# Optimization experiments

Measured on AMD Instinct MI355X. Metric: run time of the kernel, lower is better.

Reference implementation:

```python
import jax, jax.numpy as jnp
import numpy as np

B, N, T, D, O = 8, 1024, 12, 64, 64

def setup_inputs() -> dict:
    key = jax.random.key(0)
    k1, k2, k3 = jax.random.split(key, 3)
    x = jax.random.normal(k1, (B, N, T, D), dtype=jnp.float32)
    # row-normalized random adjacency (dense mask, as in the torch module)
    adj = jax.random.uniform(k2, (N, N), dtype=jnp.float32)
    norm_adj = adj / jnp.sum(adj, axis=-1, keepdims=True)
    theta_w = jax.random.normal(k3, (D, O), dtype=jnp.float32) / np.sqrt(D)
    return {"x": x, "norm_adj": norm_adj, "theta_w": theta_w}

def reference(x, norm_adj, theta_w):
    b, n, t, d = x.shape
    # [B, N, T, D] -> [B*T, N, D]
    xr = jnp.transpose(x, (0, 2, 1, 3)).reshape(b * t, n, d)
    # spatial attention scores [B*T, N, N]
    scores = jnp.einsum('gnd,gmd->gnm', xr, xr) / jnp.sqrt(jnp.float32(d))
    attn = jax.nn.softmax(scores, axis=-1)
    # adjacency-masked attention, then aggregate and project
    agg = jnp.einsum('gnm,gmd->gnd', norm_adj[None, :, :] * attn, xr)
    out = jnp.einsum('gnd,do->gno', agg, theta_w)
    # [B*T, N, O] -> [B, N, T, O], relu
    out = jnp.transpose(out.reshape(b, t, n, -1), (0, 2, 1, 3))
    return jax.nn.relu(out)
```

## Files before the change

### kernel.cpp

```cpp
#include <hip/hip_runtime.h>


#define NB    8
#define NT    12
#define NNODE 1024
#define ND    64
#define XROW  768

typedef __bf16 bf16x8 __attribute__((ext_vector_type(8)));
typedef float  floatx4 __attribute__((ext_vector_type(4)));

#define MFMA(a,b,c) __builtin_amdgcn_mfma_f32_16x16x32_bf16((a),(b),(c),0,0,0)

#define QSCALE 0.18033688011112042f

#define KSTRIDE 72
#define VSTRIDE 40
#define PSTRIDE 36
#define AGSTRIDE 68
#define OFF_KHI 0
#define OFF_KLO 4608
#define OFF_VHI 9216
#define OFF_VLO 14336
#define OFF_P   19456
#define SMEM_BYTES (19456 + 128*PSTRIDE*4)

struct bfpair { __bf16 h, l; };

__device__ __forceinline__ bfpair split1(float f) {
    bfpair r;
    __bf16 hb = (__bf16)f;
    float hf = __builtin_bit_cast(float,
                   (unsigned)__builtin_bit_cast(unsigned short, hb) << 16);
    r.h = hb;
    r.l = (__bf16)(f - hf);
    return r;
}

__global__ void __launch_bounds__(256, 2)
spattn(const float* __restrict__ x, const float* __restrict__ adj,
       const float* __restrict__ theta, float* __restrict__ out)
{
    __shared__ __align__(16) char smem[SMEM_BYTES];
    __bf16* Khi = (__bf16*)(smem + OFF_KHI);
    __bf16* Klo = (__bf16*)(smem + OFF_KLO);
    __bf16* Vhi = (__bf16*)(smem + OFF_VHI);
    __bf16* Vlo = (__bf16*)(smem + OFF_VLO);
    float*  Pm  = (float*)(smem + OFF_P);

    const int tid  = threadIdx.x;
    const int wave = tid >> 6;
    const int lane = tid & 63;
    const int l16  = lane & 15;
    const int quad = lane >> 4;

    const int bx   = blockIdx.x;
    const int g    = bx >> 3;
    const int rblk = bx & 7;
    const int bb   = g / NT;
    const int tt   = g - bb * NT;
    const int row0 = rblk * 128;

    const float* xbase = x + (size_t)bb * (NNODE * XROW) + tt * ND;

    bf16x8 qhi[2][2], qlo[2][2];
    #pragma unroll
    for (int mt = 0; mt < 2; ++mt) {
        const float* qsrc = xbase + (size_t)(row0 + wave*32 + mt*16 + l16) * XROW;
        #pragma unroll
        for (int ks = 0; ks < 2; ++ks) {
            floatx4 f0 = *(const floatx4*)(qsrc + ks*32 + quad*8);
            floatx4 f1 = *(const floatx4*)(qsrc + ks*32 + quad*8 + 4);
            #pragma unroll
            for (int i = 0; i < 4; ++i) {
                bfpair p0 = split1(f0[i]*QSCALE);
                qhi[mt][ks][i]   = p0.h; qlo[mt][ks][i]   = p0.l;
                bfpair p1 = split1(f1[i]*QSCALE);
                qhi[mt][ks][4+i] = p1.h; qlo[mt][ks][4+i] = p1.l;
            }
        }
    }

    const floatx4 vzero = {0.f, 0.f, 0.f, 0.f};
    floatx4 acc[2][4];
    #pragma unroll
    for (int mt = 0; mt < 2; ++mt)
        #pragma unroll
        for (int dt = 0; dt < 4; ++dt)
            acc[mt][dt] = vzero;
    float lpart[2][4] = {{0.f,0.f,0.f,0.f},{0.f,0.f,0.f,0.f}};

    const int skey = tid >> 3;
    const int sd0  = (tid & 7) * 8;
    const int svd  = tid >> 2;
    const int svk0 = (tid & 3) * 8;
    floatx4 kf0, kf1;
    float vf[8];

    {
        const float* ksrc = xbase + (size_t)skey * XROW + sd0;
        kf0 = *(const floatx4*)ksrc;
        kf1 = *(const floatx4*)(ksrc + 4);
        const float* vsrc = xbase + (size_t)svk0 * XROW + svd;
        #pragma unroll
        for (int i = 0; i < 8; ++i) vf[i] = vsrc[i * XROW];
    }

    for (int ct = 0; ct < 32; ++ct) {
        const int key0 = ct * 32;
        __syncthreads();
        {
            bf16x8 h, l;
            #pragma unroll
            for (int i = 0; i < 4; ++i) {
                bfpair p0 = split1(kf0[i]); h[i]   = p0.h; l[i]   = p0.l;
                bfpair p1 = split1(kf1[i]); h[4+i] = p1.h; l[4+i] = p1.l;
            }
            *(bf16x8*)(Khi + skey*KSTRIDE + sd0) = h;
            *(bf16x8*)(Klo + skey*KSTRIDE + sd0) = l;
            bf16x8 vh, vl;
            #pragma unroll
            for (int i = 0; i < 8; ++i) {
                bfpair p = split1(vf[i]); vh[i] = p.h; vl[i] = p.l;
            }
            *(bf16x8*)(Vhi + svd*VSTRIDE + svk0) = vh;
            *(bf16x8*)(Vlo + svd*VSTRIDE + svk0) = vl;
        }
        __syncthreads();
        if (ct < 31) {
            const int nk = key0 + 32;
            const float* ksrc = xbase + (size_t)(nk + skey) * XROW + sd0;
            kf0 = *(const floatx4*)ksrc;
            kf1 = *(const floatx4*)(ksrc + 4);
            const float* vsrc = xbase + (size_t)(nk + svk0) * XROW + svd;
            #pragma unroll
            for (int i = 0; i < 8; ++i) vf[i] = vsrc[i * XROW];
        }
        float av[2][2][4];
        #pragma unroll
        for (int mt = 0; mt < 2; ++mt)
            #pragma unroll
            for (int nt = 0; nt < 2; ++nt)
                #pragma unroll
                for (int r = 0; r < 4; ++r)
                    av[mt][nt][r] = adj[(size_t)(row0 + wave*32 + mt*16 + quad*4 + r) * NNODE
                                        + key0 + nt*16 + l16];

        floatx4 S[2][2] = {{vzero, vzero}, {vzero, vzero}};
        #pragma unroll
        for (int ks = 0; ks < 2; ++ks) {
            #pragma unroll
            for (int nt = 0; nt < 2; ++nt) {
                bf16x8 bh = *(const bf16x8*)(Khi + (nt*16 + l16)*KSTRIDE + ks*32 + quad*8);
                bf16x8 bl = *(const bf16x8*)(Klo + (nt*16 + l16)*KSTRIDE + ks*32 + quad*8);
                #pragma unroll
                for (int mt = 0; mt < 2; ++mt) {
                    S[mt][nt] = MFMA(qhi[mt][ks], bh, S[mt][nt]);
                    S[mt][nt] = MFMA(qlo[mt][ks], bh, S[mt][nt]);
                    S[mt][nt] = MFMA(qhi[mt][ks], bl, S[mt][nt]);
                }
            }
        }
        #pragma unroll
        for (int mt = 0; mt < 2; ++mt)
            #pragma unroll
            for (int nt = 0; nt < 2; ++nt)
                #pragma unroll
                for (int r = 0; r < 4; ++r) {
                    float w = __builtin_amdgcn_exp2f(S[mt][nt][r]);
                    lpart[mt][r] += w;
                    Pm[(wave*32 + mt*16 + quad*4 + r)*PSTRIDE + nt*16 + l16] = av[mt][nt][r] * w;
                }
        bf16x8 pah[2], pal[2];
        #pragma unroll
        for (int mt = 0; mt < 2; ++mt) {
            const float* pp = Pm + (wave*32 + mt*16 + l16)*PSTRIDE + quad*8;
            floatx4 p0 = *(const floatx4*)pp;
            floatx4 p1 = *(const floatx4*)(pp + 4);
            #pragma unroll
            for (int i = 0; i < 4; ++i) {
                bfpair q0 = split1(p0[i]); pah[mt][i]   = q0.h; pal[mt][i]   = q0.l;
                bfpair q1 = split1(p1[i]); pah[mt][4+i] = q1.h; pal[mt][4+i] = q1.l;
            }
        }
        #pragma unroll
        for (int dt = 0; dt < 4; ++dt) {
            bf16x8 vh = *(const bf16x8*)(Vhi + (dt*16 + l16)*VSTRIDE + quad*8);
            bf16x8 vl = *(const bf16x8*)(Vlo + (dt*16 + l16)*VSTRIDE + quad*8);
            #pragma unroll
            for (int mt = 0; mt < 2; ++mt) {
                acc[mt][dt] = MFMA(pah[mt], vh, acc[mt][dt]);
                acc[mt][dt] = MFMA(pal[mt], vh, acc[mt][dt]);
                acc[mt][dt] = MFMA(pah[mt], vl, acc[mt][dt]);
            }
        }
    }

    float linv[2][4];
    #pragma unroll
    for (int mt = 0; mt < 2; ++mt)
        #pragma unroll
        for (int r = 0; r < 4; ++r) {
            float lv = lpart[mt][r];
            lv += __shfl_xor(lv, 1);
            lv += __shfl_xor(lv, 2);
            lv += __shfl_xor(lv, 4);
            lv += __shfl_xor(lv, 8);
            linv[mt][r] = 1.0f / lv;
        }

    __syncthreads();
    float* AG = (float*)smem;
    #pragma unroll
    for (int mt = 0; mt < 2; ++mt)
        #pragma unroll
        for (int dt = 0; dt < 4; ++dt)
            #pragma unroll
            for (int r = 0; r < 4; ++r)
                AG[(wave*32 + mt*16 + quad*4 + r)*AGSTRIDE + dt*16 + l16]
                    = acc[mt][dt][r] * linv[mt][r];

    bf16x8 th[4][2], tl[4][2];
    #pragma unroll
    for (int ot = 0; ot < 4; ++ot)
        #pragma unroll
        for (int ks = 0; ks < 2; ++ks)
            #pragma unroll
            for (int j = 0; j < 8; ++j) {
                float tv = theta[(ks*32 + quad*8 + j)*ND + ot*16 + l16];
                bfpair p = split1(tv);
                th[ot][ks][j] = p.h; tl[ot][ks][j] = p.l;
            }

    floatx4 oacc[2][4];
    #pragma unroll
    for (int mt = 0; mt < 2; ++mt)
        #pragma unroll
        for (int ot = 0; ot < 4; ++ot)
            oacc[mt][ot] = vzero;
    __syncthreads();
    #pragma unroll
    for (int ks = 0; ks < 2; ++ks) {
        bf16x8 ah[2], al[2];
        #pragma unroll
        for (int mt = 0; mt < 2; ++mt) {
            const float* ap = AG + (wave*32 + mt*16 + l16)*AGSTRIDE + ks*32 + quad*8;
            floatx4 a0 = *(const floatx4*)ap;
            floatx4 a1 = *(const floatx4*)(ap + 4);
            #pragma unroll
            for (int i = 0; i < 4; ++i) {
                bfpair q0 = split1(a0[i]); ah[mt][i]   = q0.h; al[mt][i]   = q0.l;
                bfpair q1 = split1(a1[i]); ah[mt][4+i] = q1.h; al[mt][4+i] = q1.l;
            }
        }
        #pragma unroll
        for (int ot = 0; ot < 4; ++ot)
            #pragma unroll
            for (int mt = 0; mt < 2; ++mt) {
                oacc[mt][ot] = MFMA(ah[mt], th[ot][ks], oacc[mt][ot]);
                oacc[mt][ot] = MFMA(al[mt], th[ot][ks], oacc[mt][ot]);
                oacc[mt][ot] = MFMA(ah[mt], tl[ot][ks], oacc[mt][ot]);
            }
    }

    float* obase = out + (size_t)bb * (NNODE * XROW) + tt * ND;
    #pragma unroll
    for (int mt = 0; mt < 2; ++mt)
        #pragma unroll
        for (int ot = 0; ot < 4; ++ot)
            #pragma unroll
            for (int r = 0; r < 4; ++r) {
                float v = oacc[mt][ot][r];
                obase[(size_t)(row0 + wave*32 + mt*16 + quad*4 + r) * XROW + ot*16 + l16]
                    = v > 0.f ? v : 0.f;
            }
}

extern "C" void kernel_launch(void* const* d_in, const int* in_sizes, int n_in,
                              void* d_out, int out_size, void* d_ws, size_t ws_size,
                              hipStream_t stream) {
    (void)in_sizes; (void)n_in; (void)d_ws; (void)ws_size; (void)out_size;
    const float* x     = (const float*)d_in[0];
    const float* adj   = (const float*)d_in[1];
    const float* theta = (const float*)d_in[2];
    float* out = (float*)d_out;
    spattn<<<dim3(768), dim3(256), 0, stream>>>(x, adj, theta, out);
}
```

Measured before the change: 171.0 us.

## Switch to transposed 32x32x16 MFMA flow with register-resident P and aggregates

Replaces the 16x16x32 MFMA tiles with 32x32x16 MFMAs that compute S transposed (keys x queries). Each lane then owns one query row, so the probability tile and the aggregated output are turned into B operands with a lane-xor-32 shuffle instead of a round trip through LDS. This removes the P and AG shared-memory buffers and their barriers in the epilogue. Adjacency and output accesses become vectorized float4 per query row. It adds shuffle and select work and increases register pressure from the floatx16 accumulators.

Result: slower. 176.2 us (+3.0%).

```diff
diff --git a/kernel.cpp b/kernel.cpp
--- a/kernel.cpp
+++ b/kernel.cpp
@@ -7,23 +7,22 @@
 #define ND    64
 #define XROW  768
 
-typedef __bf16 bf16x8 __attribute__((ext_vector_type(8)));
+typedef __bf16 bf16x8  __attribute__((ext_vector_type(8)));
+typedef __bf16 bf16x2  __attribute__((ext_vector_type(2)));
 typedef float  floatx4 __attribute__((ext_vector_type(4)));
-
-#define MFMA(a,b,c) __builtin_amdgcn_mfma_f32_16x16x32_bf16((a),(b),(c),0,0,0)
-
+typedef float  floatx16 __attribute__((ext_vector_type(16)));
+typedef unsigned uintx4 __attribute__((ext_vector_type(4)));
+
+#define MFMA32(a,b,c) __builtin_amdgcn_mfma_f32_32x32x16_bf16((a),(b),(c),0,0,0)
 #define QSCALE 0.18033688011112042f
 
 #define KSTRIDE 72
 #define VSTRIDE 40
-#define PSTRIDE 36
-#define AGSTRIDE 68
 #define OFF_KHI 0
 #define OFF_KLO 4608
 #define OFF_VHI 9216
 #define OFF_VLO 14336
-#define OFF_P   19456
-#define SMEM_BYTES (19456 + 128*PSTRIDE*4)
+#define SMEM_BYTES 19456
 
 struct bfpair { __bf16 h, l; };
 
@@ -35,6 +34,25 @@
     r.h = hb;
     r.l = (__bf16)(f - hf);
     return r;
+}
+
+__device__ __forceinline__ unsigned pk2(__bf16 a, __bf16 b) {
+    bf16x2 t; t[0] = a; t[1] = b;
+    return __builtin_bit_cast(unsigned, t);
+}
+
+__device__ __forceinline__ bf16x8 xchg(unsigned A0, unsigned A1,
+                                       unsigned B0, unsigned B1, int L5) {
+    unsigned sA = L5 ? A0 : B0;
+    unsigned sB = L5 ? A1 : B1;
+    unsigned rA = (unsigned)__shfl_xor((int)sA, 32);
+    unsigned rB = (unsigned)__shfl_xor((int)sB, 32);
+    uintx4 u;
+    u[0] = L5 ? rA : A0;
+    u[1] = L5 ? rB : A1;
+    u[2] = L5 ? B0 : rA;
+    u[3] = L5 ? B1 : rB;
+    return __builtin_bit_cast(bf16x8, u);
 }
 
 __global__ void __launch_bounds__(256, 2)
@@ -46,13 +64,12 @@
     __bf16* Klo = (__bf16*)(smem + OFF_KLO);
     __bf16* Vhi = (__bf16*)(smem + OFF_VHI);
     __bf16* Vlo = (__bf16*)(smem + OFF_VLO);
-    float*  Pm  = (float*)(smem + OFF_P);
 
     const int tid  = threadIdx.x;
     const int wave = tid >> 6;
     const int lane = tid & 63;
-    const int l16  = lane & 15;
-    const int quad = lane >> 4;
+    const int q31  = lane & 31;
+    const int L5   = lane >> 5;
 
     const int bx   = blockIdx.x;
     const int g    = bx >> 3;
@@ -60,35 +77,30 @@
     const int bb   = g / NT;
     const int tt   = g - bb * NT;
     const int row0 = rblk * 128;
+    const int wq   = wave * 32;
+    const int qglob = row0 + wq + q31;
 
     const float* xbase = x + (size_t)bb * (NNODE * XROW) + tt * ND;
 
-    bf16x8 qhi[2][2], qlo[2][2];
-    #pragma unroll
-    for (int mt = 0; mt < 2; ++mt) {
-        const float* qsrc = xbase + (size_t)(row0 + wave*32 + mt*16 + l16) * XROW;
-        #pragma unroll
-        for (int ks = 0; ks < 2; ++ks) {
-            floatx4 f0 = *(const floatx4*)(qsrc + ks*32 + quad*8);
-            floatx4 f1 = *(const floatx4*)(qsrc + ks*32 + quad*8 + 4);
+    bf16x8 qh[4], ql[4];
+    {
+        const float* qsrc = xbase + (size_t)qglob * XROW;
+        #pragma unroll
+        for (int dc = 0; dc < 4; ++dc) {
+            floatx4 f0 = *(const floatx4*)(qsrc + dc*16 + L5*8);
+            floatx4 f1 = *(const floatx4*)(qsrc + dc*16 + L5*8 + 4);
             #pragma unroll
             for (int i = 0; i < 4; ++i) {
                 bfpair p0 = split1(f0[i]*QSCALE);
-                qhi[mt][ks][i]   = p0.h; qlo[mt][ks][i]   = p0.l;
+                qh[dc][i]   = p0.h; ql[dc][i]   = p0.l;
                 bfpair p1 = split1(f1[i]*QSCALE);
-                qhi[mt][ks][4+i] = p1.h; qlo[mt][ks][4+i] = p1.l;
-            }
-        }
-    }
-
-    const floatx4 vzero = {0.f, 0.f, 0.f, 0.f};
-    floatx4 acc[2][4];
-    #pragma unroll
-    for (int mt = 0; mt < 2; ++mt)
-        #pragma unroll
-        for (int dt = 0; dt < 4; ++dt)
-            acc[mt][dt] = vzero;
-    float lpart[2][4] = {{0.f,0.f,0.f,0.f},{0.f,0.f,0.f,0.f}};
+                qh[dc][4+i] = p1.h; ql[dc][4+i] = p1.l;
+            }
+        }
+    }
+
+    floatx16 O0 = {}, O1 = {};
+    float lpart = 0.f;
 
     const int skey = tid >> 3;
     const int sd0  = (tid & 7) * 8;
@@ -136,144 +148,123 @@
             #pragma unroll
             for (int i = 0; i < 8; ++i) vf[i] = vsrc[i * XROW];
         }
-        float av[2][2][4];
-        #pragma unroll
-        for (int mt = 0; mt < 2; ++mt)
-            #pragma unroll
-            for (int nt = 0; nt < 2; ++nt)
-                #pragma unroll
-                for (int r = 0; r < 4; ++r)
-                    av[mt][nt][r] = adj[(size_t)(row0 + wave*32 + mt*16 + quad*4 + r) * NNODE
-                                        + key0 + nt*16 + l16];
-
-        floatx4 S[2][2] = {{vzero, vzero}, {vzero, vzero}};
-        #pragma unroll
-        for (int ks = 0; ks < 2; ++ks) {
-            #pragma unroll
-            for (int nt = 0; nt < 2; ++nt) {
-                bf16x8 bh = *(const bf16x8*)(Khi + (nt*16 + l16)*KSTRIDE + ks*32 + quad*8);
-                bf16x8 bl = *(const bf16x8*)(Klo + (nt*16 + l16)*KSTRIDE + ks*32 + quad*8);
-                #pragma unroll
-                for (int mt = 0; mt < 2; ++mt) {
-                    S[mt][nt] = MFMA(qhi[mt][ks], bh, S[mt][nt]);
-                    S[mt][nt] = MFMA(qlo[mt][ks], bh, S[mt][nt]);
-                    S[mt][nt] = MFMA(qhi[mt][ks], bl, S[mt][nt]);
-                }
-            }
-        }
-        #pragma unroll
-        for (int mt = 0; mt < 2; ++mt)
-            #pragma unroll
-            for (int nt = 0; nt < 2; ++nt)
-                #pragma unroll
-                for (int r = 0; r < 4; ++r) {
-                    float w = __builtin_amdgcn_exp2f(S[mt][nt][r]);
-                    lpart[mt][r] += w;
-                    Pm[(wave*32 + mt*16 + quad*4 + r)*PSTRIDE + nt*16 + l16] = av[mt][nt][r] * w;
-                }
-        bf16x8 pah[2], pal[2];
-        #pragma unroll
-        for (int mt = 0; mt < 2; ++mt) {
-            const float* pp = Pm + (wave*32 + mt*16 + l16)*PSTRIDE + quad*8;
-            floatx4 p0 = *(const floatx4*)pp;
-            floatx4 p1 = *(const floatx4*)(pp + 4);
-            #pragma unroll
-            for (int i = 0; i < 4; ++i) {
-                bfpair q0 = split1(p0[i]); pah[mt][i]   = q0.h; pal[mt][i]   = q0.l;
-                bfpair q1 = split1(p1[i]); pah[mt][4+i] = q1.h; pal[mt][4+i] = q1.l;
-            }
-        }
-        #pragma unroll
-        for (int dt = 0; dt < 4; ++dt) {
-            bf16x8 vh = *(const bf16x8*)(Vhi + (dt*16 + l16)*VSTRIDE + quad*8);
-            bf16x8 vl = *(const bf16x8*)(Vlo + (dt*16 + l16)*VSTRIDE + quad*8);
-            #pragma unroll
-            for (int mt = 0; mt < 2; ++mt) {
-                acc[mt][dt] = MFMA(pah[mt], vh, acc[mt][dt]);
-                acc[mt][dt] = MFMA(pal[mt], vh, acc[mt][dt]);
-                acc[mt][dt] = MFMA(pah[mt], vl, acc[mt][dt]);
-            }
-        }
-    }
-
-    float linv[2][4];
-    #pragma unroll
-    for (int mt = 0; mt < 2; ++mt)
-        #pragma unroll
-        for (int r = 0; r < 4; ++r) {
-            float lv = lpart[mt][r];
-            lv += __shfl_xor(lv, 1);
-            lv += __shfl_xor(lv, 2);
-            lv += __shfl_xor(lv, 4);
-            lv += __shfl_xor(lv, 8);
-            linv[mt][r] = 1.0f / lv;
-        }
-
-    __syncthreads();
-    float* AG = (float*)smem;
-    #pragma unroll
-    for (int mt = 0; mt < 2; ++mt)
-        #pragma unroll
-        for (int dt = 0; dt < 4; ++dt)
-            #pragma unroll
-            for (int r = 0; r < 4; ++r)
-                AG[(wave*32 + mt*16 + quad*4 + r)*AGSTRIDE + dt*16 + l16]
-                    = acc[mt][dt][r] * linv[mt][r];
-
-    bf16x8 th[4][2], tl[4][2];
-    #pragma unroll
-    for (int ot = 0; ot < 4; ++ot)
-        #pragma unroll
-        for (int ks = 0; ks < 2; ++ks)
+        floatx4 adjv[4];
+        #pragma unroll
+        for (int rg = 0; rg < 4; ++rg)
+            adjv[rg] = *(const floatx4*)(adj + (size_t)qglob * NNODE
+                                         + key0 + rg*8 + L5*4);
+
+        floatx16 ST = {};
+        #pragma unroll
+        for (int dc = 0; dc < 4; ++dc) {
+            bf16x8 kh = *(const bf16x8*)(Khi + q31*KSTRIDE + dc*16 + L5*8);
+            bf16x8 kl = *(const bf16x8*)(Klo + q31*KSTRIDE + dc*16 + L5*8);
+            ST = MFMA32(kh, qh[dc], ST);
+            ST = MFMA32(kl, qh[dc], ST);
+            ST = MFMA32(kh, ql[dc], ST);
+        }
+        __bf16 pth[16], ptl[16];
+        #pragma unroll
+        for (int r = 0; r < 16; ++r) {
+            float w = __builtin_amdgcn_exp2f(ST[r]);
+            lpart += w;
+            bfpair p = split1(adjv[r >> 2][r & 3] * w);
+            pth[r] = p.h; ptl[r] = p.l;
+        }
+        unsigned GH[4][2], GL[4][2];
+        #pragma unroll
+        for (int gg = 0; gg < 4; ++gg) {
+            GH[gg][0] = pk2(pth[4*gg],   pth[4*gg+1]);
+            GH[gg][1] = pk2(pth[4*gg+2], pth[4*gg+3]);
+            GL[gg][0] = pk2(ptl[4*gg],   ptl[4*gg+1]);
+            GL[gg][1] = pk2(ptl[4*gg+2], ptl[4*gg+3]);
+        }
+        #pragma unroll
+        for (int kc = 0; kc < 2; ++kc) {
+            bf16x8 bh = xchg(GH[2*kc][0], GH[2*kc][1],
+                             GH[2*kc+1][0], GH[2*kc+1][1], L5);
+            bf16x8 bl = xchg(GL[2*kc][0], GL[2*kc][1],
+                             GL[2*kc+1][0], GL[2*kc+1][1], L5);
+            {
+                bf16x8 vh = *(const bf16x8*)(Vhi + q31*VSTRIDE + kc*16 + L5*8);
+                bf16x8 vl = *(const bf16x8*)(Vlo + q31*VSTRIDE + kc*16 + L5*8);
+                O0 = MFMA32(vh, bh, O0);
+                O0 = MFMA32(vl, bh, O0);
+                O0 = MFMA32(vh, bl, O0);
+            }
+            {
+                bf16x8 vh = *(const bf16x8*)(Vhi + (32+q31)*VSTRIDE + kc*16 + L5*8);
+                bf16x8 vl = *(const bf16x8*)(Vlo + (32+q31)*VSTRIDE + kc*16 + L5*8);
+                O1 = MFMA32(vh, bh, O1);
+                O1 = MFMA32(vl, bh, O1);
+                O1 = MFMA32(vh, bl, O1);
+            }
+        }
+    }
+
+    float l = lpart + __shfl_xor(lpart, 32);
+    float linv = 1.0f / l;
+
+    bf16x8 th[2][4], tlo[2][4];
+    #pragma unroll
+    for (int ot = 0; ot < 2; ++ot)
+        #pragma unroll
+        for (int kc = 0; kc < 4; ++kc)
             #pragma unroll
             for (int j = 0; j < 8; ++j) {
-                float tv = theta[(ks*32 + quad*8 + j)*ND + ot*16 + l16];
+                float tv = theta[(size_t)(kc*16 + L5*8 + j) * ND + ot*32 + q31];
                 bfpair p = split1(tv);
-                th[ot][ks][j] = p.h; tl[ot][ks][j] = p.l;
-            }
-
-    floatx4 oacc[2][4];
-    #pragma unroll
-    for (int mt = 0; mt < 2; ++mt)
-        #pragma unroll
-        for (int ot = 0; ot < 4; ++ot)
-            oacc[mt][ot] = vzero;
-    __syncthreads();
-    #pragma unroll
-    for (int ks = 0; ks < 2; ++ks) {
-        bf16x8 ah[2], al[2];
-        #pragma unroll
-        for (int mt = 0; mt < 2; ++mt) {
-            const float* ap = AG + (wave*32 + mt*16 + l16)*AGSTRIDE + ks*32 + quad*8;
-            floatx4 a0 = *(const floatx4*)ap;
-            floatx4 a1 = *(const floatx4*)(ap + 4);
-            #pragma unroll
-            for (int i = 0; i < 4; ++i) {
-                bfpair q0 = split1(a0[i]); ah[mt][i]   = q0.h; al[mt][i]   = q0.l;
-                bfpair q1 = split1(a1[i]); ah[mt][4+i] = q1.h; al[mt][4+i] = q1.l;
-            }
-        }
-        #pragma unroll
-        for (int ot = 0; ot < 4; ++ot)
-            #pragma unroll
-            for (int mt = 0; mt < 2; ++mt) {
-                oacc[mt][ot] = MFMA(ah[mt], th[ot][ks], oacc[mt][ot]);
-                oacc[mt][ot] = MFMA(al[mt], th[ot][ks], oacc[mt][ot]);
-                oacc[mt][ot] = MFMA(ah[mt], tl[ot][ks], oacc[mt][ot]);
-            }
-    }
-
-    float* obase = out + (size_t)bb * (NNODE * XROW) + tt * ND;
-    #pragma unroll
-    for (int mt = 0; mt < 2; ++mt)
-        #pragma unroll
-        for (int ot = 0; ot < 4; ++ot)
-            #pragma unroll
-            for (int r = 0; r < 4; ++r) {
-                float v = oacc[mt][ot][r];
-                obase[(size_t)(row0 + wave*32 + mt*16 + quad*4 + r) * XROW + ot*16 + l16]
-                    = v > 0.f ? v : 0.f;
-            }
+                th[ot][kc][j] = p.h; tlo[ot][kc][j] = p.l;
+            }
+
+    __bf16 agh[32], agl[32];
+    #pragma unroll
+    for (int r = 0; r < 16; ++r) {
+        bfpair p = split1(O0[r] * linv);
+        agh[r] = p.h; agl[r] = p.l;
+    }
+    #pragma unroll
+    for (int r = 0; r < 16; ++r) {
+        bfpair p = split1(O1[r] * linv);
+        agh[16+r] = p.h; agl[16+r] = p.l;
+    }
+    unsigned AH[8][2], AL[8][2];
+    #pragma unroll
+    for (int gg = 0; gg < 8; ++gg) {
+        AH[gg][0] = pk2(agh[4*gg],   agh[4*gg+1]);
+        AH[gg][1] = pk2(agh[4*gg+2], agh[4*gg+3]);
+        AL[gg][0] = pk2(agl[4*gg],   agl[4*gg+1]);
+        AL[gg][1] = pk2(agl[4*gg+2], agl[4*gg+3]);
+    }
+
+    floatx16 OC0 = {}, OC1 = {};
+    #pragma unroll
+    for (int kc = 0; kc < 4; ++kc) {
+        bf16x8 bh = xchg(AH[2*kc][0], AH[2*kc][1],
+                         AH[2*kc+1][0], AH[2*kc+1][1], L5);
+        bf16x8 bl = xchg(AL[2*kc][0], AL[2*kc][1],
+                         AL[2*kc+1][0], AL[2*kc+1][1], L5);
+        OC0 = MFMA32(th[0][kc], bh, OC0);
+        OC0 = MFMA32(tlo[0][kc], bh, OC0);
+        OC0 = MFMA32(th[0][kc], bl, OC0);
+        OC1 = MFMA32(th[1][kc], bh, OC1);
+        OC1 = MFMA32(tlo[1][kc], bh, OC1);
+        OC1 = MFMA32(th[1][kc], bl, OC1);
+    }
+
+    float* obase = out + (size_t)bb * (NNODE * XROW) + tt * ND
+                       + (size_t)qglob * XROW;
+    #pragma unroll
+    for (int rg = 0; rg < 4; ++rg) {
+        floatx4 v0, v1;
+        #pragma unroll
+        for (int i = 0; i < 4; ++i) {
+            float a = OC0[4*rg + i]; v0[i] = a > 0.f ? a : 0.f;
+            float b = OC1[4*rg + i]; v1[i] = b > 0.f ? b : 0.f;
+        }
+        *(floatx4*)(obase + 8*rg + 4*L5)      = v0;
+        *(floatx4*)(obase + 32 + 8*rg + 4*L5) = v1;
+    }
 }
 
 extern "C" void kernel_launch(void* const* d_in, const int* in_sizes, int n_in,
```
